# Performance work log

Hardware: AMD Instinct MI355X
Metric: run time of the kernel (lower is better)

Reference implementation:

```python
import jax, jax.numpy as jnp
import numpy as np

B, C, N = 16, 256, 2048
DA = C // 4
BN_EPS = 1e-5


def setup_inputs() -> dict:
    key = jax.random.key(0)
    ks = jax.random.split(key, 7)
    s = lambda fan_in: 1.0 / np.sqrt(fan_in)
    return {
        "x": jax.random.normal(ks[0], (B, C, N), dtype=jnp.float32),
        "Wq": jax.random.normal(ks[1], (DA, C), dtype=jnp.float32) * s(C),
        "Wk": jax.random.normal(ks[2], (DA, C), dtype=jnp.float32) * s(C),
        "Wv": jax.random.normal(ks[3], (C, C), dtype=jnp.float32) * s(C),
        "Wp": jax.random.normal(ks[4], (C, C), dtype=jnp.float32) * s(C),
        "gamma": jnp.ones((C,), dtype=jnp.float32),
        "beta": jnp.zeros((C,), dtype=jnp.float32),
    }


def reference(x, Wq, Wk, Wv, Wp, gamma, beta):
    # 1x1 conv projections (pointwise over N)
    q = jnp.einsum("dc,bcn->bnd", Wq, x)          # [B, N, da]
    k = jnp.einsum("dc,bcm->bdm", Wk, x)          # [B, da, N]
    v = jnp.einsum("oc,bcm->bmo", Wv, x)          # [B, N, C]

    energy = jnp.einsum("bnd,bdm->bnm", q, k)     # [B, N, N]
    # offset-attention double normalization: softmax over query axis (dim=1),
    # then L1 renormalization over key axis (dim=-1)
    attn = jax.nn.softmax(energy, axis=1)
    attn = attn / (1e-9 + attn.sum(axis=-1, keepdims=True))

    fsa = jnp.einsum("bnm,bmo->bon", attn, v)     # [B, C, N]

    # proj: Conv1d(1x1, no bias) -> BatchNorm1d (training-mode batch stats) -> ReLU
    y = x - fsa
    h = jnp.einsum("oc,bcn->bon", Wp, y)          # [B, C, N]
    mean = h.mean(axis=(0, 2), keepdims=True)
    var = h.var(axis=(0, 2), keepdims=True)       # biased variance
    h = (h - mean) * jax.lax.rsqrt(var + BN_EPS)
    h = h * gamma[None, :, None] + beta[None, :, None]
    h = jax.nn.relu(h)
    return h + x
```

## Files before the change

### kernel.cpp

```cpp
#include <hip/hip_runtime.h>
#include <math.h>

#define B_ 16
#define C_ 256
#define N_ 2048
#define D_ 64
#define NP_ 2080

typedef __attribute__((ext_vector_type(8))) short bf8;
typedef __attribute__((ext_vector_type(4))) float f4;

#define MFMA16(A, Bv, Cv) __builtin_amdgcn_mfma_f32_16x16x32_bf16(A, Bv, Cv, 0, 0, 0)

__device__ __forceinline__ short f2b(float f) {
  unsigned u = __float_as_uint(f);
  u = (u + 0x7fff + ((u >> 16) & 1)) >> 16;
  return (short)u;
}
__device__ __forceinline__ float b2f(short s) {
  return __uint_as_float(((unsigned)(unsigned short)s) << 16);
}

static constexpr size_t OFF_XT = 0;
static constexpr size_t OFF_QN = (size_t)16 << 20;
static constexpr size_t OFF_KN = (size_t)20 << 20;
static constexpr size_t OFF_VT = (size_t)24 << 20;
static constexpr size_t OFF_CI = (size_t)42 << 20;
static constexpr size_t OFF_WQ = OFF_CI + ((size_t)128 << 10);
static constexpr size_t OFF_WK = OFF_WQ + ((size_t)32 << 10);
static constexpr size_t OFF_WV = OFF_WK + ((size_t)32 << 10);
static constexpr size_t OFF_WP = OFF_WV + ((size_t)128 << 10);
static constexpr size_t OFF_S1 = OFF_WP + ((size_t)128 << 10);
static constexpr size_t OFF_S2 = OFF_S1 + 1024;
static constexpr size_t OFF_P1 = OFF_S2 + 4096;
static constexpr size_t OFF_P2 = OFF_P1 + ((size_t)512 << 10);

__global__ __launch_bounds__(256) void transpose_x_kernel(
    const float* __restrict__ x, short* __restrict__ xT,
    const float* __restrict__ fq, const float* __restrict__ fk,
    const float* __restrict__ fv, const float* __restrict__ fp,
    short* __restrict__ wq, short* __restrict__ wk,
    short* __restrict__ wv, short* __restrict__ wp) {
  if (blockIdx.z == 16) {
    int idx = (blockIdx.y * 32 + blockIdx.x) * 256 + threadIdx.x;
#pragma unroll
    for (int r = 0; r < 5; ++r) {
      int e = idx + r * 32768;
      if (e < 16384) wq[e] = f2b(fq[e]);
      else if (e < 32768) wk[e - 16384] = f2b(fk[e - 16384]);
      else if (e < 98304) wv[e - 32768] = f2b(fv[e - 32768]);
      else if (e < 163840) wp[e - 98304] = f2b(fp[e - 98304]);
    }
    return;
  }
  __shared__ float t[64][65];
  const int b = blockIdx.z, c0 = blockIdx.y * 64, n0 = blockIdx.x * 64;
  const int tid = threadIdx.x;
  const float* xp = x + ((size_t)b * C_ + c0) * N_ + n0;
#pragma unroll
  for (int i = 0; i < 16; ++i) {
    int idx = tid + i * 256;
    int cl = idx >> 6, nl = idx & 63;
    t[cl][nl] = xp[(size_t)cl * N_ + nl];
  }
  __syncthreads();
  short* op = xT + ((size_t)b * N_ + n0) * C_ + c0;
#pragma unroll
  for (int i = 0; i < 8; ++i) {
    int idx = tid + i * 256;
    int nl = idx >> 5, cl2 = (idx & 31) * 2;
    ushort2 v;
    v.x = (unsigned short)f2b(t[cl2][nl]);
    v.y = (unsigned short)f2b(t[cl2 + 1][nl]);
    *(ushort2*)(op + (size_t)nl * C_ + cl2) = v;
  }
}

__global__ __launch_bounds__(256, 4) void proj_all_kernel(
    const short* __restrict__ xT, const short* __restrict__ Wqb,
    const short* __restrict__ Wkb, const short* __restrict__ Wvb,
    short* __restrict__ Qn, short* __restrict__ Kn, short* __restrict__ Vt) {
  const int tid = threadIdx.x;
  const int wv = tid >> 6, lane = tid & 63;
  const int li = lane & 15, quad = lane >> 4;
  const int z = blockIdx.z;
  const short* W;
  short* out;
  int o0;
  bool outt;
  if (z == 0) { W = Wqb; out = Qn; o0 = 0; outt = true; }
  else if (z == 1) { W = Wkb; out = Kn; o0 = 0; outt = true; }
  else { W = Wvb; out = Vt; o0 = (z - 2) * 64; outt = false; }
  const int b = blockIdx.y, n0 = blockIdx.x * 64;
  const int n = n0 + wv * 16 + li;
  const short* xrow = xT + ((size_t)b * N_ + n) * C_ + quad * 8;
  f4 acc[4] = {};
  for (int ks = 0; ks < 8; ++ks) {
    bf8 bfr = *(const bf8*)(xrow + ks * 32);
#pragma unroll
    for (int ot = 0; ot < 4; ++ot) {
      bf8 afr = *(const bf8*)(W + (size_t)(o0 + ot * 16 + li) * C_ + ks * 32 + quad * 8);
      acc[ot] = MFMA16(afr, bfr, acc[ot]);
    }
  }
  if (outt) {
#pragma unroll
    for (int ot = 0; ot < 4; ++ot) {
      short4 v = {f2b(acc[ot].x), f2b(acc[ot].y), f2b(acc[ot].z), f2b(acc[ot].w)};
      *(short4*)(out + ((size_t)b * N_ + n) * D_ + ot * 16 + quad * 4) = v;
    }
  } else {
#pragma unroll
    for (int ot = 0; ot < 4; ++ot) {
#pragma unroll
      for (int r = 0; r < 4; ++r) {
        out[((size_t)b * C_ + o0 + ot * 16 + quad * 4 + r) * NP_ + n] = f2b(acc[ot][r]);
      }
    }
  }
}

__global__ __launch_bounds__(256, 2) void colstats_kernel(const short* __restrict__ Qn,
                                                          const short* __restrict__ Kn,
                                                          float* __restrict__ cinv) {
  __shared__ short qS[2][64][72];
  const int tid = threadIdx.x;
  const int wv = tid >> 6, lane = tid & 63;
  const int li = lane & 15, quad = lane >> 4;
  const int b = blockIdx.y, m0 = blockIdx.x * 64;
  const short* krow = Kn + ((size_t)b * N_ + m0 + wv * 16 + li) * D_ + quad * 8;
  bf8 af0 = *(const bf8*)(krow);
  bf8 af1 = *(const bf8*)(krow + 32);
  const short* Qb = Qn + (size_t)b * N_ * D_;
#pragma unroll
  for (int j = 0; j < 2; ++j) {
    int idx = tid * 2 + j;
    int row = idx >> 3, c8 = (idx & 7) * 8;
    *(bf8*)&qS[0][row][c8] = *(const bf8*)(Qb + (size_t)row * D_ + c8);
  }
  __syncthreads();
  float csum[4] = {0.f, 0.f, 0.f, 0.f};
  for (int t = 0; t < 32; ++t) {
    if (t < 31) {
#pragma unroll
      for (int j = 0; j < 2; ++j) {
        int idx = tid * 2 + j;
        int row = idx >> 3, c8 = (idx & 7) * 8;
        *(bf8*)&qS[(t + 1) & 1][row][c8] =
            *(const bf8*)(Qb + (size_t)((t + 1) * 64 + row) * D_ + c8);
      }
    }
#pragma unroll
    for (int nt = 0; nt < 4; ++nt) {
      bf8 b0 = *(const bf8*)&qS[t & 1][nt * 16 + li][quad * 8];
      bf8 b1 = *(const bf8*)&qS[t & 1][nt * 16 + li][32 + quad * 8];
      f4 s = {};
      s = MFMA16(af0, b0, s);
      s = MFMA16(af1, b1, s);
      csum[0] += __expf(s.x);
      csum[1] += __expf(s.y);
      csum[2] += __expf(s.z);
      csum[3] += __expf(s.w);
    }
    __syncthreads();
  }
#pragma unroll
  for (int r = 0; r < 4; ++r) {
#pragma unroll
    for (int m = 1; m < 16; m <<= 1) csum[r] += __shfl_xor(csum[r], m);
  }
  if (li == 0) {
#pragma unroll
    for (int r = 0; r < 4; ++r)
      cinv[(size_t)b * N_ + m0 + wv * 16 + quad * 4 + r] = 1.f / csum[r];
  }
}

__global__ __launch_bounds__(512, 2) void attn_fsa_kernel(
    const float* __restrict__ x, const short* __restrict__ Qn, const short* __restrict__ Kn,
    const short* __restrict__ Vt, const float* __restrict__ cinv, short* __restrict__ yT) {
  __shared__ short pT[2][64][136];
  __shared__ float civS[2048];
  __shared__ float racc[64];
  const int tid = threadIdx.x;
  const int wv = tid >> 6, lane = tid & 63;
  const int li = lane & 15, quad = lane >> 4;
  const int b = blockIdx.y, n0 = blockIdx.x * 64;
  *(float4*)(civS + tid * 4) = *(const float4*)(cinv + (size_t)b * N_ + tid * 4);
  if (tid < 64) racc[tid] = 0.f;
  bf8 q[4][2];
#pragma unroll
  for (int nt = 0; nt < 4; ++nt) {
    const short* qrow = Qn + ((size_t)b * N_ + n0 + nt * 16 + li) * D_ + quad * 8;
    q[nt][0] = *(const bf8*)(qrow);
    q[nt][1] = *(const bf8*)(qrow + 32);
  }
  __syncthreads();
  f4 acc[2][4] = {};
  float rloc[4] = {};
  const int ob = wv * 32;
  const short* Kb = Kn + (size_t)b * N_ * D_;
  const short* Vb = Vt + (size_t)b * C_ * NP_;
  {
    const short* krow = Kb + (size_t)(wv * 16 + li) * D_ + quad * 8;
    bf8 a0 = *(const bf8*)(krow);
    bf8 a1 = *(const bf8*)(krow + 32);
    f4 civ4 = *(const f4*)(civS + wv * 16 + quad * 4);
#pragma unroll
    for (int nt = 0; nt < 4; ++nt) {
      f4 s = {};
      s = MFMA16(a0, q[nt][0], s);
      s = MFMA16(a1, q[nt][1], s);
      short4 pv;
#pragma unroll
      for (int r = 0; r < 4; ++r) {
        float p = __expf(s[r]) * civ4[r];
        short ph = f2b(p);
        ((short*)&pv)[r] = ph;
        rloc[nt] += b2f(ph);
      }
      *(short4*)&pT[0][nt * 16 + li][wv * 16 + quad * 4] = pv;
    }
  }
  bf8 va[2][4];
#pragma unroll
  for (int ot = 0; ot < 2; ++ot)
#pragma unroll
    for (int kf = 0; kf < 4; ++kf)
      va[ot][kf] = *(const bf8*)(Vb + (size_t)(ob + ot * 16 + li) * NP_ + kf * 32 + quad * 8);
  __syncthreads();
  for (int t = 0; t < 16; ++t) {
    const int mm2 = (t + 1) * 128;
    bf8 vn[2][4], a0, a1;
    if (t < 15) {
#pragma unroll
      for (int ot = 0; ot < 2; ++ot)
#pragma unroll
        for (int kf = 0; kf < 4; ++kf)
          vn[ot][kf] = *(const bf8*)(Vb + (size_t)(ob + ot * 16 + li) * NP_ +
                                     mm2 + kf * 32 + quad * 8);
      const short* krow = Kb + (size_t)(mm2 + wv * 16 + li) * D_ + quad * 8;
      a0 = *(const bf8*)(krow);
      a1 = *(const bf8*)(krow + 32);
    }
    const short* Pb = &pT[t & 1][0][0];
#pragma unroll
    for (int nt = 0; nt < 4; ++nt) {
#pragma unroll
      for (int kf = 0; kf < 4; ++kf) {
        bf8 pb = *(const bf8*)(Pb + (size_t)(nt * 16 + li) * 136 + kf * 32 + quad * 8);
#pragma unroll
        for (int ot = 0; ot < 2; ++ot) acc[ot][nt] = MFMA16(va[ot][kf], pb, acc[ot][nt]);
      }
    }
    if (t < 15) {
      f4 civ4 = *(const f4*)(civS + mm2 + wv * 16 + quad * 4);
      short* Pw = &pT[(t + 1) & 1][0][0];
#pragma unroll
      for (int nt = 0; nt < 4; ++nt) {
        f4 s = {};
        s = MFMA16(a0, q[nt][0], s);
        s = MFMA16(a1, q[nt][1], s);
        short4 pv;
#pragma unroll
        for (int r = 0; r < 4; ++r) {
          float p = __expf(s[r]) * civ4[r];
          short ph = f2b(p);
          ((short*)&pv)[r] = ph;
          rloc[nt] += b2f(ph);
        }
        *(short4*)(Pw + (size_t)(nt * 16 + li) * 136 + wv * 16 + quad * 4) = pv;
      }
#pragma unroll
      for (int ot = 0; ot < 2; ++ot)
#pragma unroll
        for (int kf = 0; kf < 4; ++kf) va[ot][kf] = vn[ot][kf];
    }
    __syncthreads();
  }
#pragma unroll
  for (int nt = 0; nt < 4; ++nt) {
    float rv = rloc[nt];
    rv += __shfl_xor(rv, 16);
    rv += __shfl_xor(rv, 32);
    if (quad == 0) atomicAdd(&racc[nt * 16 + li], rv);
  }
  __syncthreads();
#pragma unroll
  for (int nt = 0; nt < 4; ++nt) {
    const int nn = n0 + nt * 16 + li;
    const float rinv = 1.f / (1e-9f + racc[nt * 16 + li]);
    short* yrow = yT + ((size_t)b * N_ + nn) * C_ + ob;
#pragma unroll
    for (int ot = 0; ot < 2; ++ot) {
      short4 v;
#pragma unroll
      for (int r = 0; r < 4; ++r) {
        int o = ob + ot * 16 + quad * 4 + r;
        float xv = x[((size_t)b * C_ + o) * N_ + nn];
        ((short*)&v)[r] = f2b(xv - acc[ot][nt][r] * rinv);
      }
      *(short4*)(yrow + ot * 16 + quad * 4) = v;
    }
  }
}

__global__ __launch_bounds__(256, 4) void wp_kernel(const short* __restrict__ yT,
                                                    const short* __restrict__ Wp,
                                                    float* __restrict__ H,
                                                    float* __restrict__ P1,
                                                    float* __restrict__ P2) {
  __shared__ alignas(16) float ha[64][68];
  __shared__ float red1[64][4];
  __shared__ float red2[64][4];
  const int tid = threadIdx.x;
  const int wv = tid >> 6, lane = tid & 63;
  const int li = lane & 15, quad = lane >> 4;
  const int b = blockIdx.y, n0 = blockIdx.x * 64, o0 = blockIdx.z * 64;
  const int n = n0 + wv * 16 + li;
  const short* yrow = yT + ((size_t)b * N_ + n) * C_ + quad * 8;
  f4 acc[4] = {};
  for (int ks = 0; ks < 8; ++ks) {
    bf8 bfr = *(const bf8*)(yrow + ks * 32);
#pragma unroll
    for (int ot = 0; ot < 4; ++ot) {
      bf8 afr = *(const bf8*)(Wp + (size_t)(o0 + ot * 16 + li) * C_ + ks * 32 + quad * 8);
      acc[ot] = MFMA16(afr, bfr, acc[ot]);
    }
  }
#pragma unroll
  for (int ot = 0; ot < 4; ++ot)
#pragma unroll
    for (int r = 0; r < 4; ++r) ha[ot * 16 + quad * 4 + r][wv * 16 + li] = acc[ot][r];
  __syncthreads();
  const int o = tid >> 2, nq = tid & 3;
  float s1p = 0.f, s2p = 0.f;
  float* hrow = H + ((size_t)b * C_ + o0 + o) * N_ + n0 + nq * 16;
#pragma unroll
  for (int j4 = 0; j4 < 4; ++j4) {
    float4 v = *reinterpret_cast<const float4*>(&ha[o][nq * 16 + j4 * 4]);
    s1p += v.x + v.y + v.z + v.w;
    s2p += v.x * v.x + v.y * v.y + v.z * v.z + v.w * v.w;
    reinterpret_cast<float4*>(hrow)[j4] = v;
  }
  red1[o][nq] = s1p;
  red2[o][nq] = s2p;
  __syncthreads();
  if (tid < 64) {
    float a1 = red1[tid][0] + red1[tid][1] + red1[tid][2] + red1[tid][3];
    float a2 = red2[tid][0] + red2[tid][1] + red2[tid][2] + red2[tid][3];
    const int g = b * 32 + blockIdx.x;
    P1[(size_t)g * 256 + o0 + tid] = a1;
    P2[(size_t)g * 256 + o0 + tid] = a2;
  }
}

__global__ __launch_bounds__(256) void bn_reduce_kernel(const float* __restrict__ P1,
                                                        const float* __restrict__ P2,
                                                        float* __restrict__ S1,
                                                        float* __restrict__ S2) {
  const int lc = threadIdx.x >> 4, gl = threadIdx.x & 15;
  const int c = blockIdx.x * 16 + lc;
  float a1 = 0.f, a2 = 0.f;
#pragma unroll
  for (int k = 0; k < 32; ++k) {
    int g = gl + k * 16;
    a1 += P1[(size_t)g * 256 + c];
    a2 += P2[(size_t)g * 256 + c];
  }
#pragma unroll
  for (int m = 1; m < 16; m <<= 1) {
    a1 += __shfl_xor(a1, m);
    a2 += __shfl_xor(a2, m);
  }
  if (gl == 0) {
    S1[c] = a1;
    S2[c] = a2;
  }
}

__global__ __launch_bounds__(256) void bn_apply_kernel(const float* __restrict__ H,
                                                       const float* __restrict__ x,
                                                       const float* __restrict__ S1,
                                                       const float* __restrict__ S2,
                                                       const float* __restrict__ gamma,
                                                       const float* __restrict__ beta,
                                                       float* __restrict__ out) {
  size_t idx = ((size_t)blockIdx.x * 256 + threadIdx.x) * 4;
  int o = (int)((idx >> 11) & 255);
  const float invn = 1.f / ((float)B_ * N_);
  float mean = S1[o] * invn;
  float var = S2[o] * invn - mean * mean;
  float inv = rsqrtf(var + 1e-5f);
  float a = gamma[o] * inv;
  float c = beta[o] - mean * a;
  float4 h = *reinterpret_cast<const float4*>(&H[idx]);
  float4 xv = *reinterpret_cast<const float4*>(&x[idx]);
  float4 r;
  r.x = fmaxf(h.x * a + c, 0.f) + xv.x;
  r.y = fmaxf(h.y * a + c, 0.f) + xv.y;
  r.z = fmaxf(h.z * a + c, 0.f) + xv.z;
  r.w = fmaxf(h.w * a + c, 0.f) + xv.w;
  *reinterpret_cast<float4*>(&out[idx]) = r;
}

extern "C" void kernel_launch(void* const* d_in, const int* in_sizes, int n_in,
                              void* d_out, int out_size, void* d_ws, size_t ws_size,
                              hipStream_t stream) {
  (void)in_sizes; (void)n_in; (void)out_size; (void)ws_size;
  const float* x = (const float*)d_in[0];
  const float* Wq = (const float*)d_in[1];
  const float* Wk = (const float*)d_in[2];
  const float* Wv = (const float*)d_in[3];
  const float* Wp = (const float*)d_in[4];
  const float* gamma = (const float*)d_in[5];
  const float* beta = (const float*)d_in[6];
  char* ws = (char*)d_ws;
  short* xT = (short*)(ws + OFF_XT);
  short* Qn = (short*)(ws + OFF_QN);
  short* Kn = (short*)(ws + OFF_KN);
  short* Vt = (short*)(ws + OFF_VT);
  float* CI = (float*)(ws + OFF_CI);
  short* Wqb = (short*)(ws + OFF_WQ);
  short* Wkb = (short*)(ws + OFF_WK);
  short* Wvb = (short*)(ws + OFF_WV);
  short* Wpb = (short*)(ws + OFF_WP);
  float* S1 = (float*)(ws + OFF_S1);
  float* S2 = (float*)(ws + OFF_S2);
  float* P1 = (float*)(ws + OFF_P1);
  float* P2 = (float*)(ws + OFF_P2);
  short* yT = xT;
  float* out = (float*)d_out;
  float* H = out;

  dim3 blk(256);
  transpose_x_kernel<<<dim3(32, 4, 17), blk, 0, stream>>>(x, xT, Wq, Wk, Wv, Wp,
                                                          Wqb, Wkb, Wvb, Wpb);
  proj_all_kernel<<<dim3(32, 16, 6), blk, 0, stream>>>(xT, Wqb, Wkb, Wvb, Qn, Kn, Vt);
  colstats_kernel<<<dim3(32, 16), blk, 0, stream>>>(Qn, Kn, CI);
  attn_fsa_kernel<<<dim3(32, 16), dim3(512), 0, stream>>>(x, Qn, Kn, Vt, CI, yT);
  wp_kernel<<<dim3(32, 16, 4), blk, 0, stream>>>(yT, Wpb, H, P1, P2);
  bn_reduce_kernel<<<dim3(16), blk, 0, stream>>>(P1, P2, S1, S2);
  bn_apply_kernel<<<dim3(8192), blk, 0, stream>>>(H, x, S1, S2, gamma, beta, out);
}
```

Baseline: 308.0 us.

## Prefetch K two tiles ahead and stagger S/PV phases across waves

K fragments for the score tile are now loaded two iterations ahead instead of one, so more latency is hidden. Odd waves run the PV MFMAs before the next tile's score/exp work and even waves do the reverse, so the exp-heavy and MFMA-heavy phases of different waves overlap on the compute unit. The score computation is moved into a lambda shared by the prologue and the loop. The cost is extra registers for the deeper K prefetch, which could lower occupancy.

New measurement: 322.1 us. 4.6% more time.

```diff
diff --git a/kernel.cpp b/kernel.cpp
--- a/kernel.cpp
+++ b/kernel.cpp
@@ -201,11 +201,10 @@
   const int ob = wv * 32;
   const short* Kb = Kn + (size_t)b * N_ * D_;
   const short* Vb = Vt + (size_t)b * C_ * NP_;
-  {
-    const short* krow = Kb + (size_t)(wv * 16 + li) * D_ + quad * 8;
-    bf8 a0 = *(const bf8*)(krow);
-    bf8 a1 = *(const bf8*)(krow + 32);
-    f4 civ4 = *(const f4*)(civS + wv * 16 + quad * 4);
+
+  auto do_s = [&](int t1, bf8 a0, bf8 a1) {
+    f4 civ4 = *(const f4*)(civS + t1 * 128 + wv * 16 + quad * 4);
+    short* Pw = &pT[t1 & 1][0][0];
 #pragma unroll
     for (int nt = 0; nt < 4; ++nt) {
       f4 s = {};
@@ -219,8 +218,15 @@
         ((short*)&pv)[r] = ph;
         rloc[nt] += b2f(ph);
       }
-      *(short4*)&pT[0][nt * 16 + li][wv * 16 + quad * 4] = pv;
-    }
+      *(short4*)(Pw + (size_t)(nt * 16 + li) * 136 + wv * 16 + quad * 4) = pv;
+    }
+  };
+
+  {
+    const short* krow = Kb + (size_t)(wv * 16 + li) * D_ + quad * 8;
+    bf8 a0 = *(const bf8*)(krow);
+    bf8 a1 = *(const bf8*)(krow + 32);
+    do_s(0, a0, a1);
   }
   bf8 va[2][4];
 #pragma unroll
@@ -228,10 +234,17 @@
 #pragma unroll
     for (int kf = 0; kf < 4; ++kf)
       va[ot][kf] = *(const bf8*)(Vb + (size_t)(ob + ot * 16 + li) * NP_ + kf * 32 + quad * 8);
-  __syncthreads();
+  bf8 ka0, ka1;
+  {
+    const short* krow = Kb + (size_t)(128 + wv * 16 + li) * D_ + quad * 8;
+    ka0 = *(const bf8*)(krow);
+    ka1 = *(const bf8*)(krow + 32);
+  }
+  __syncthreads();
+
   for (int t = 0; t < 16; ++t) {
     const int mm2 = (t + 1) * 128;
-    bf8 vn[2][4], a0, a1;
+    bf8 vn[2][4], kn0, kn1;
     if (t < 15) {
 #pragma unroll
       for (int ot = 0; ot < 2; ++ot)
@@ -239,42 +252,40 @@
         for (int kf = 0; kf < 4; ++kf)
           vn[ot][kf] = *(const bf8*)(Vb + (size_t)(ob + ot * 16 + li) * NP_ +
                                      mm2 + kf * 32 + quad * 8);
-      const short* krow = Kb + (size_t)(mm2 + wv * 16 + li) * D_ + quad * 8;
-      a0 = *(const bf8*)(krow);
-      a1 = *(const bf8*)(krow + 32);
-    }
-    const short* Pb = &pT[t & 1][0][0];
-#pragma unroll
-    for (int nt = 0; nt < 4; ++nt) {
-#pragma unroll
-      for (int kf = 0; kf < 4; ++kf) {
-        bf8 pb = *(const bf8*)(Pb + (size_t)(nt * 16 + li) * 136 + kf * 32 + quad * 8);
-#pragma unroll
-        for (int ot = 0; ot < 2; ++ot) acc[ot][nt] = MFMA16(va[ot][kf], pb, acc[ot][nt]);
+    }
+    if (t < 14) {
+      const short* krow = Kb + (size_t)((t + 2) * 128 + wv * 16 + li) * D_ + quad * 8;
+      kn0 = *(const bf8*)(krow);
+      kn1 = *(const bf8*)(krow + 32);
+    }
+    auto do_pv = [&]() {
+      const short* Pb = &pT[t & 1][0][0];
+#pragma unroll
+      for (int nt = 0; nt < 4; ++nt) {
+#pragma unroll
+        for (int kf = 0; kf < 4; ++kf) {
+          bf8 pb = *(const bf8*)(Pb + (size_t)(nt * 16 + li) * 136 + kf * 32 + quad * 8);
+#pragma unroll
+          for (int ot = 0; ot < 2; ++ot) acc[ot][nt] = MFMA16(va[ot][kf], pb, acc[ot][nt]);
+        }
       }
+    };
+    if (wv & 1) {
+      do_pv();
+      if (t < 15) do_s(t + 1, ka0, ka1);
+    } else {
+      if (t < 15) do_s(t + 1, ka0, ka1);
+      do_pv();
     }
     if (t < 15) {
-      f4 civ4 = *(const f4*)(civS + mm2 + wv * 16 + quad * 4);
-      short* Pw = &pT[(t + 1) & 1][0][0];
-#pragma unroll
-      for (int nt = 0; nt < 4; ++nt) {
-        f4 s = {};
-        s = MFMA16(a0, q[nt][0], s);
-        s = MFMA16(a1, q[nt][1], s);
-        short4 pv;
-#pragma unroll
-        for (int r = 0; r < 4; ++r) {
-          float p = __expf(s[r]) * civ4[r];
-          short ph = f2b(p);
-          ((short*)&pv)[r] = ph;
-          rloc[nt] += b2f(ph);
-        }
-        *(short4*)(Pw + (size_t)(nt * 16 + li) * 136 + wv * 16 + quad * 4) = pv;
-      }
 #pragma unroll
       for (int ot = 0; ot < 2; ++ot)
 #pragma unroll
         for (int kf = 0; kf < 4; ++kf) va[ot][kf] = vn[ot][kf];
+    }
+    if (t < 14) {
+      ka0 = kn0;
+      ka1 = kn1;
     }
     __syncthreads();
   }
```
